# Kernel optimization log

Hardware: AMD Instinct MI355X
Metric: run time of the kernel (lower is better)

Reference implementation:

```python
import jax, jax.numpy as jnp
import numpy as np

N = 8192
E = 262144
NEG = 0.2  # leaky_relu negative slope used throughout


def setup_inputs() -> dict:
    key = jax.random.key(0)
    def rn(i, shape, s=0.05):
        return jax.random.normal(jax.random.fold_in(key, i), shape, jnp.float32) * s
    d = {}
    d["x"] = jax.random.normal(jax.random.fold_in(key, 0), (N, 64), jnp.float32)
    d["edge_index"] = jax.random.randint(jax.random.fold_in(key, 1), (2, E), 0, N, dtype=jnp.int32)
    wshapes = {"w0": (64, 256), "as0": (4, 64), "ad0": (4, 64), "r0": (64, 256),
               "w1": (256, 256), "as1": (4, 64), "ad1": (4, 64), "r1": (256, 256),
               "w2": (256, 64), "as2": (1, 64), "ad2": (1, 64), "r2": (256, 64),
               "p0": (256, 64), "p1": (256, 64),
               "qw": (64, 64), "kw": (64, 64), "vw": (64, 64), "ow": (64, 64),
               "m1w": (64, 64), "m2w": (64, 32), "m3w": (32, 10)}
    for i, (nm, sh) in enumerate(wshapes.items()):
        d[nm] = rn(i + 2, sh)
    for nm, dim in [("g0", 256), ("g1", 256), ("g2", 64)]:
        d[nm] = jnp.ones((dim,), jnp.float32)
    for nm, dim in [("be0", 256), ("be1", 256), ("be2", 64), ("b0", 256), ("b1", 256), ("b2", 64),
                    ("qb", 64), ("kb", 64), ("vb", 64), ("ob", 64), ("m1b", 64), ("m2b", 32), ("m3b", 10)]:
        d[nm] = jnp.zeros((dim,), jnp.float32)
    return d


def _forward(edge_index, x, w0, as0, ad0, b0, g0, be0, r0,
             w1, as1, ad1, b1, g1, be1, r1,
             w2, as2, ad2, b2, g2, be2, r2,
             p0, p1, qw, qb, kw, kb, vw, vb, ow, ob,
             m1w, m1b, m2w, m2b, m3w, m3b):
    n = x.shape[0]
    loops = jnp.arange(n, dtype=edge_index.dtype)
    src = jnp.concatenate([edge_index[0], loops])  # add_self_loops=True
    dst = jnp.concatenate([edge_index[1], loops])

    def gat(h, w, a_s, a_d, b, heads):
        hw = (h @ w).reshape(n, heads, 64)  # [N, H, C]
        # PyG GATConv: e_ij = leaky_relu(att_src . h_j + att_dst . h_i), softmax over in-edges of i
        e = jax.nn.leaky_relu(jnp.sum(hw * a_s, -1)[src] + jnp.sum(hw * a_d, -1)[dst], NEG)  # [Etot, H]
        m = jax.ops.segment_max(e, dst, num_segments=n)
        ex = jnp.exp(e - m[dst])
        den = jax.ops.segment_sum(ex, dst, num_segments=n)
        alpha = ex / (den[dst] + 1e-16)
        out = jax.ops.segment_sum(hw[src] * alpha[:, :, None], dst, num_segments=n)
        return out.reshape(n, heads * 64) + b

    def bn(h, g, bta):  # BatchNorm1d, batch statistics (training-mode math)
        mu = jnp.mean(h, 0)
        var = jnp.var(h, 0)
        return (h - mu) * jax.lax.rsqrt(var + 1e-5) * g + bta

    outs = []
    h = x
    for (w, a_s, a_d, b, g, bt, r, heads) in [
            (w0, as0, ad0, b0, g0, be0, r0, 4),
            (w1, as1, ad1, b1, g1, be1, r1, 4),
            (w2, as2, ad2, b2, g2, be2, r2, 1)]:
        res = h @ r
        h = bn(gat(h, w, a_s, a_d, b, heads), g, bt) + res  # shapes always match here
        h = jax.nn.leaky_relu(h, NEG)
        outs.append(h)

    # JumpingKnowledge 'max' after projecting first two layers to hidden dim
    z = jnp.maximum(jnp.maximum(outs[0] @ p0, outs[1] @ p1), outs[2])  # [N, 64]

    # MultiHeadSelfAttention over all nodes (batch=1 implicit), 2 heads, head_dim=32
    q = (z @ qw + qb).reshape(n, 2, 32)
    k = (z @ kw + kb).reshape(n, 2, 32)
    v = (z @ vw + vb).reshape(n, 2, 32)
    attn = jax.nn.softmax(jnp.einsum('nhd,mhd->hnm', q, k) * (32 ** -0.5), axis=-1)
    z = jnp.einsum('hnm,mhd->nhd', attn, v).reshape(n, 64) @ ow + ob

    # MLP head (no data.batch -> GlobalAttention pool skipped)
    z = jax.nn.leaky_relu(z @ m1w + m1b, NEG)
    z = jax.nn.leaky_relu(z @ m2w + m2b, NEG)
    return z @ m3w + m3b


def reference(x, edge_index, w0, as0, ad0, b0, g0, be0, r0,
              w1, as1, ad1, b1, g1, be1, r1,
              w2, as2, ad2, b2, g2, be2, r2,
              p0, p1, qw, qb, kw, kb, vw, vb, ow, ob,
              m1w, m1b, m2w, m2b, m3w, m3b):
    return _forward(edge_index, x, w0, as0, ad0, b0, g0, be0, r0,
                    w1, as1, ad1, b1, g1, be1, r1,
                    w2, as2, ad2, b2, g2, be2, r2,
                    p0, p1, qw, qb, kw, kb, vw, vb, ow, ob,
                    m1w, m1b, m2w, m2b, m3w, m3b)
```

## Files before the change

kernel.cpp:

```cpp
#include <hip/hip_runtime.h>
#include <hip/hip_bf16.h>


#define NEG 0.2f

__device__ __forceinline__ float leaky(float v) { return v > 0.f ? v : NEG * v; }

__device__ __forceinline__ unsigned bf16u(float x) {
    unsigned u = __float_as_uint(x);
    u += 0x7FFFu + ((u >> 16) & 1u);
    return u >> 16;
}

typedef __attribute__((ext_vector_type(8))) short bf16x8;
typedef __attribute__((ext_vector_type(16))) float f32x16;
typedef __attribute__((ext_vector_type(4))) unsigned uint4v;

__device__ __forceinline__ void split1(float v, unsigned& hb, unsigned& lb) {
    hb = bf16u(v);
    float hf = __uint_as_float(hb << 16);
    lb = bf16u(v - hf);
}

__global__ void split_rows(const float* __restrict__ in,
                           unsigned short* __restrict__ hi,
                           unsigned short* __restrict__ lo, int total4)
{
    int i = blockIdx.x * 256 + threadIdx.x;
    if (i >= total4) return;
    float4 v = ((const float4*)in)[i];
    float vv[4] = {v.x, v.y, v.z, v.w};
    ushort4 h, l;
#pragma unroll
    for (int j = 0; j < 4; ++j) {
        unsigned hb, lb;
        split1(vv[j], hb, lb);
        (&h.x)[j] = (unsigned short)hb;
        (&l.x)[j] = (unsigned short)lb;
    }
    ((ushort4*)hi)[i] = h;
    ((ushort4*)lo)[i] = l;
}

struct WEnt { const float* src; unsigned short* hi; unsigned short* lo; int K; int N; };
struct WArr { WEnt e[15]; };

__global__ void split_weights(WArr a)
{
    WEnt w = a.e[blockIdx.y];
    int id = blockIdx.x * 256 + threadIdx.x;
    if (id >= w.K * w.N) return;
    int k = id / w.N, n = id - k * w.N;
    unsigned hb, lb;
    split1(w.src[id], hb, lb);
    w.hi[(size_t)n * w.K + k] = (unsigned short)hb;
    w.lo[(size_t)n * w.K + k] = (unsigned short)lb;
}

__global__ __launch_bounds__(256) void gemm_mfma(
    const unsigned short* __restrict__ Ahi, const unsigned short* __restrict__ Alo,
    const unsigned short* __restrict__ Bhi, const unsigned short* __restrict__ Blo,
    const float* __restrict__ bias, float* __restrict__ C,
    unsigned short* __restrict__ Chi, unsigned short* __restrict__ Clo,
    int M, int N, int K, int act)
{
    const int lane = threadIdx.x & 63, wid = threadIdx.x >> 6;
    const int hb4 = lane >> 5, lq = lane & 31;
    const int row0 = blockIdx.y * 64 + (wid >> 1) * 32;
    const int col0 = blockIdx.x * 64 + (wid & 1) * 32;
    const size_t abase = (size_t)(row0 + lq) * K + hb4 * 8;
    const size_t bbase = (size_t)(col0 + lq) * K + hb4 * 8;
    f32x16 acc0, acc1;
#pragma unroll
    for (int r = 0; r < 16; ++r) { acc0[r] = 0.f; acc1[r] = 0.f; }
    for (int k0 = 0; k0 < K; k0 += 16) {
        bf16x8 a_h = *(const bf16x8*)(Ahi + abase + k0);
        bf16x8 a_l = *(const bf16x8*)(Alo + abase + k0);
        bf16x8 b_h = *(const bf16x8*)(Bhi + bbase + k0);
        bf16x8 b_l = *(const bf16x8*)(Blo + bbase + k0);
        acc0 = __builtin_amdgcn_mfma_f32_32x32x16_bf16(a_h, b_h, acc0, 0, 0, 0);
        acc1 = __builtin_amdgcn_mfma_f32_32x32x16_bf16(a_l, b_h, acc1, 0, 0, 0);
        acc1 = __builtin_amdgcn_mfma_f32_32x32x16_bf16(a_h, b_l, acc1, 0, 0, 0);
    }
    int col = col0 + lq;
    if (col >= N) return;
    float bs = bias ? bias[col] : 0.f;
#pragma unroll
    for (int r = 0; r < 16; ++r) {
        int row = row0 + (r & 3) + 8 * (r >> 2) + 4 * hb4;
        float v = acc0[r] + acc1[r] + bs;
        if (act) v = leaky(v);
        C[(size_t)row * N + col] = v;
        if (Chi) {
            unsigned hh, ll;
            split1(v, hh, ll);
            Chi[(size_t)row * N + col] = (unsigned short)hh;
            Clo[(size_t)row * N + col] = (unsigned short)ll;
        }
    }
}

__global__ void sd_kernel(const float* __restrict__ hw, const float* __restrict__ a_s,
                          const float* __restrict__ a_d, float* __restrict__ sval,
                          float* __restrict__ dval, int Nn, int H)
{
    int i = blockIdx.x * blockDim.x + threadIdx.x;
    if (i >= Nn * H) return;
    int n = i / H, h = i - n * H;
    const float4* row = (const float4*)(hw + (size_t)n * H * 64 + h * 64);
    const float4* as4 = (const float4*)(a_s + h * 64);
    const float4* ad4 = (const float4*)(a_d + h * 64);
    float s = 0.f, d = 0.f;
#pragma unroll
    for (int c = 0; c < 16; ++c) {
        float4 x = row[c], a = as4[c], b = ad4[c];
        s += x.x * a.x + x.y * a.y + x.z * a.z + x.w * a.w;
        d += x.x * b.x + x.y * b.y + x.z * b.z + x.w * b.w;
    }
    sval[i] = s;
    dval[i] = d;
}

__global__ void csr_count(const int* __restrict__ ei, int* __restrict__ cnt, int E) {
    int i = blockIdx.x * 256 + threadIdx.x;
    if (i < E) atomicAdd(&cnt[ei[E + i]], 1);
}

__global__ __launch_bounds__(256) void csr_scan(const int* __restrict__ cnt,
                                                int* __restrict__ rowptr,
                                                int* __restrict__ fill, int Nn)
{
    __shared__ int part[256];
    int t = threadIdx.x;
    int loc[32];
    int s = 0;
#pragma unroll
    for (int j = 0; j < 32; ++j) { loc[j] = s; s += cnt[t * 32 + j]; }
    part[t] = s;
    __syncthreads();
    for (int d = 1; d < 256; d <<= 1) {
        int v = (t >= d) ? part[t - d] : 0;
        __syncthreads();
        part[t] += v;
        __syncthreads();
    }
    int off = (t > 0) ? part[t - 1] : 0;
#pragma unroll
    for (int j = 0; j < 32; ++j) {
        int v = off + loc[j];
        rowptr[t * 32 + j] = v;
        fill[t * 32 + j] = v;
    }
    if (t == 255) rowptr[Nn] = part[255];
}

__global__ void csr_scatter(const int* __restrict__ ei, int* __restrict__ fill,
                            int* __restrict__ srcidx, int E) {
    int i = blockIdx.x * 256 + threadIdx.x;
    if (i < E) {
        int d = ei[E + i];
        int p = atomicAdd(&fill[d], 1);
        srcidx[p] = ei[i];
    }
}

template <int H>
__global__ __launch_bounds__(256) void gat_gather(
    const int* __restrict__ rowptr, const int* __restrict__ srcidx,
    const float* __restrict__ hw, const float* __restrict__ sval,
    const float* __restrict__ dval, float* __restrict__ gout, int Nn)
{
    const int node = blockIdx.x * 4 + (threadIdx.x >> 6);
    const int lane = threadIdx.x & 63;
    const int beg = rowptr[node], end = rowptr[node + 1];
    const int C = H * 64;
    float dv[H], es[H], mh[H], lh[H], inv[H], acc[H];
#pragma unroll
    for (int h = 0; h < H; ++h) {
        dv[h] = dval[node * H + h];
        es[h] = leaky(sval[node * H + h] + dv[h]);
        mh[h] = -1e30f;
        lh[h] = 0.f;
    }
    for (int i = beg + lane; i < end; i += 64) {
        int s = srcidx[i];
#pragma unroll
        for (int h = 0; h < H; ++h)
            mh[h] = fmaxf(mh[h], leaky(sval[s * H + h] + dv[h]));
    }
#pragma unroll
    for (int h = 0; h < H; ++h) {
        float m = mh[h];
        for (int off = 32; off; off >>= 1) m = fmaxf(m, __shfl_xor(m, off));
        mh[h] = fmaxf(m, es[h]);
    }
    for (int i = beg + lane; i < end; i += 64) {
        int s = srcidx[i];
#pragma unroll
        for (int h = 0; h < H; ++h)
            lh[h] += __expf(leaky(sval[s * H + h] + dv[h]) - mh[h]);
    }
#pragma unroll
    for (int h = 0; h < H; ++h) {
        float l = lh[h];
        for (int off = 32; off; off >>= 1) l += __shfl_xor(l, off);
        l += __expf(es[h] - mh[h]);
        inv[h] = 1.f / (l + 1e-16f);
        acc[h] = __expf(es[h] - mh[h]) * inv[h] *
                 hw[(size_t)node * C + h * 64 + lane];
    }
    for (int i = beg; i < end; ++i) {
        int s = srcidx[i];
#pragma unroll
        for (int h = 0; h < H; ++h) {
            float e = leaky(sval[s * H + h] + dv[h]);
            float a = __expf(e - mh[h]) * inv[h];
            acc[h] += a * hw[(size_t)s * C + h * 64 + lane];
        }
    }
#pragma unroll
    for (int h = 0; h < H; ++h)
        gout[(size_t)node * C + h * 64 + lane] = acc[h];
}

__global__ void bn_partial(const float* __restrict__ gout, double* __restrict__ sums,
                           int Nn, int C)
{
    int t = threadIdx.x;
    int c = t % C, sub = t / C, nsub = blockDim.x / C;
    int rbase = blockIdx.x * 32;
    double s = 0.0, sq = 0.0;
    for (int r = rbase + sub; r < rbase + 32; r += nsub) {
        float x = gout[(size_t)r * C + c];
        s += x;
        sq += (double)x * x;
    }
    atomicAdd(&sums[c], s);
    atomicAdd(&sums[C + c], sq);
}

__global__ void bn_finalize(const double* __restrict__ sums, float* __restrict__ mu,
                            float* __restrict__ rstd, int Nn, int C)
{
    int c = threadIdx.x;
    if (c >= C) return;
    double m = sums[c] / Nn;
    double v = sums[C + c] / Nn - m * m;
    mu[c] = (float)m;
    rstd[c] = (float)(1.0 / sqrt(v + 1e-5));
}

__global__ void bn_res_act(const float* __restrict__ gout, const float* __restrict__ res,
                           const float* __restrict__ mu, const float* __restrict__ rstd,
                           const float* __restrict__ g, const float* __restrict__ be,
                           float* __restrict__ out,
                           unsigned short* __restrict__ shi,
                           unsigned short* __restrict__ slo, int total, int C)
{
    int i = blockIdx.x * blockDim.x + threadIdx.x;
    if (i >= total) return;
    int c = i & (C - 1);
    float v = (gout[i] - mu[c]) * rstd[c] * g[c] + be[c] + res[i];
    v = leaky(v);
    out[i] = v;
    if (shi) {
        unsigned hb, lb;
        split1(v, hb, lb);
        shi[i] = (unsigned short)hb;
        slo[i] = (unsigned short)lb;
    }
}

__global__ void jk_max(const float* __restrict__ a, const float* __restrict__ b,
                       const float* __restrict__ c, float* __restrict__ z,
                       unsigned short* __restrict__ shi,
                       unsigned short* __restrict__ slo, int total)
{
    int i = blockIdx.x * blockDim.x + threadIdx.x;
    if (i >= total) return;
    float v = fmaxf(fmaxf(a[i], b[i]), c[i]);
    z[i] = v;
    unsigned hb, lb;
    split1(v, hb, lb);
    shi[i] = (unsigned short)hb;
    slo[i] = (unsigned short)lb;
}

__global__ void kmax_kernel(const float* __restrict__ kg, unsigned* __restrict__ kmax,
                            int N)
{
    const int c = threadIdx.x & 63, g = threadIdx.x >> 6;
    const int rows = N / (gridDim.x * 4);
    const int r0 = (blockIdx.x * 4 + g) * rows;
    float m = 0.f;
    for (int r = r0; r < r0 + rows; ++r)
        m = fmaxf(m, fabsf(kg[(size_t)r * 64 + c]));
    atomicMax(&kmax[c], __float_as_uint(m));
}

__global__ void qk_prep(const float* __restrict__ zq, const float* __restrict__ zk,
                        const unsigned* __restrict__ kmaxu,
                        __hip_bfloat16* __restrict__ Qb, __hip_bfloat16* __restrict__ Kb,
                        float* __restrict__ bound, int N)
{
    int idx = blockIdx.x * 256 + threadIdx.x;
    if (idx >= 2 * N) return;
    int h = idx / N, row = idx - h * N;
    const float scale = 0.17677669529663687f;
    const float* qp = zq + (size_t)row * 64 + h * 32;
    const float* kp = zk + (size_t)row * 64 + h * 32;
    float b = 0.f;
    unsigned qo[16], ko[16];
#pragma unroll
    for (int i = 0; i < 16; ++i) {
        float q0 = qp[2 * i] * scale, q1 = qp[2 * i + 1] * scale;
        float k0 = kp[2 * i], k1 = kp[2 * i + 1];
        b += fabsf(q0) * __uint_as_float(kmaxu[h * 32 + 2 * i]);
        b += fabsf(q1) * __uint_as_float(kmaxu[h * 32 + 2 * i + 1]);
        qo[i] = bf16u(q0) | (bf16u(q1) << 16);
        ko[i] = bf16u(k0) | (bf16u(k1) << 16);
    }
    uint4* qd = (uint4*)(Qb + (size_t)idx * 32);
    uint4* kd = (uint4*)(Kb + (size_t)idx * 32);
#pragma unroll
    for (int i = 0; i < 4; ++i) {
        qd[i] = make_uint4(qo[4 * i], qo[4 * i + 1], qo[4 * i + 2], qo[4 * i + 3]);
        kd[i] = make_uint4(ko[4 * i], ko[4 * i + 1], ko[4 * i + 2], ko[4 * i + 3]);
    }
    bound[idx] = b;
}

__global__ void v_prep(const float* __restrict__ zv, __hip_bfloat16* __restrict__ Vf,
                       int N)
{
    int idx = blockIdx.x * 256 + threadIdx.x;
    int total = 2 * (N >> 4) * 64;
    if (idx >= total) return;
    int lane = idx & 63;
    int g = (idx >> 6) % (N >> 4);
    int h = (idx >> 6) / (N >> 4);
    int kb = g * 16 + (lane >> 5) * 8;
    int d = (lane & 31) + h * 32;
    unsigned o[4];
#pragma unroll
    for (int i = 0; i < 4; ++i) {
        unsigned u0 = bf16u(zv[(size_t)(kb + 2 * i) * 64 + d]);
        unsigned u1 = bf16u(zv[(size_t)(kb + 2 * i + 1) * 64 + d]);
        o[i] = u0 | (u1 << 16);
    }
    *(uint4*)(Vf + (size_t)idx * 8) = make_uint4(o[0], o[1], o[2], o[3]);
}

__global__ __launch_bounds__(256) void attn_mfma(
    const __hip_bfloat16* __restrict__ Qb, const __hip_bfloat16* __restrict__ Kb,
    const __hip_bfloat16* __restrict__ Vf, const float* __restrict__ bound,
    float* __restrict__ pl, __hip_bfloat16* __restrict__ pacc,
    int N, int nchunk, int chunksz)
{
    const int lane = threadIdx.x & 63;
    const int wid = threadIdx.x >> 6;
    const int hi = lane >> 5, lq = lane & 31;
    const int chunk = blockIdx.x;
    const int qtile = blockIdx.y * 4 + wid;
    const int head = qtile / (N >> 5);
    const int q0 = (qtile % (N >> 5)) * 32;
    const int kbase = chunk * chunksz;

    const size_t qrow = (size_t)head * N + q0 + lq;
    const bf16x8 qf0 = *(const bf16x8*)(Qb + qrow * 32 + hi * 8);
    const bf16x8 qf1 = *(const bf16x8*)(Qb + qrow * 32 + hi * 8 + 16);
    const float bnd = bound[qrow];

    f32x16 oacc;
#pragma unroll
    for (int r = 0; r < 16; ++r) oacc[r] = 0.f;
    float lsum = 0.f;

    for (int kt = kbase; kt < kbase + chunksz; kt += 32) {
        const size_t krow = (size_t)head * N + kt + lq;
        const bf16x8 kf0 = *(const bf16x8*)(Kb + krow * 32 + hi * 8);
        const bf16x8 kf1 = *(const bf16x8*)(Kb + krow * 32 + hi * 8 + 16);
        f32x16 s;
#pragma unroll
        for (int r = 0; r < 16; ++r) s[r] = 0.f;
        s = __builtin_amdgcn_mfma_f32_32x32x16_bf16(kf0, qf0, s, 0, 0, 0);
        s = __builtin_amdgcn_mfma_f32_32x32x16_bf16(kf1, qf1, s, 0, 0, 0);
        const __hip_bfloat16* vfb =
            Vf + (((size_t)head * (N >> 4) + (kt >> 4)) * 64 + lane) * 8;
        const bf16x8 vf0 = *(const bf16x8*)vfb;
        const bf16x8 vf1 = *(const bf16x8*)(vfb + 64 * 8);

        float p[16];
#pragma unroll
        for (int r = 0; r < 16; ++r) p[r] = __expf(s[r] - bnd);
        float ls = 0.f;
#pragma unroll
        for (int r = 0; r < 16; ++r) ls += p[r];
        lsum += ls;

        unsigned wpk[8];
#pragma unroll
        for (int i = 0; i < 8; ++i)
            wpk[i] = bf16u(p[2 * i]) | (bf16u(p[2 * i + 1]) << 16);
        unsigned wsx[8];
#pragma unroll
        for (int i = 0; i < 8; ++i) wsx[i] = (unsigned)__shfl_xor((int)wpk[i], 32);
        uint4v b1, b2;
        b1[0] = hi ? wsx[2] : wpk[0];
        b1[1] = hi ? wsx[3] : wpk[1];
        b1[2] = hi ? wpk[2] : wsx[0];
        b1[3] = hi ? wpk[3] : wsx[1];
        b2[0] = hi ? wsx[6] : wpk[4];
        b2[1] = hi ? wsx[7] : wpk[5];
        b2[2] = hi ? wpk[6] : wsx[4];
        b2[3] = hi ? wpk[7] : wsx[5];
        oacc = __builtin_amdgcn_mfma_f32_32x32x16_bf16(
            vf0, __builtin_bit_cast(bf16x8, b1), oacc, 0, 0, 0);
        oacc = __builtin_amdgcn_mfma_f32_32x32x16_bf16(
            vf1, __builtin_bit_cast(bf16x8, b2), oacc, 0, 0, 0);
    }
    lsum += __shfl_xor(lsum, 32);
    const size_t hr = (size_t)head * N + q0 + lq;
    if (hi == 0) pl[hr * nchunk + chunk] = lsum;
    __hip_bfloat16* pb = pacc + (hr * nchunk + chunk) * 32;
#pragma unroll
    for (int rg = 0; rg < 4; ++rg) {
        unsigned lo = bf16u(oacc[rg * 4 + 0]) | (bf16u(oacc[rg * 4 + 1]) << 16);
        unsigned hw2 = bf16u(oacc[rg * 4 + 2]) | (bf16u(oacc[rg * 4 + 3]) << 16);
        *(uint2*)(pb + rg * 8 + hi * 4) = make_uint2(lo, hw2);
    }
}

__global__ void attn_combine(const float* __restrict__ pl,
                             const __hip_bfloat16* __restrict__ pacc,
                             float* __restrict__ og,
                             unsigned short* __restrict__ shi,
                             unsigned short* __restrict__ slo, int N, int nchunk)
{
    int i = blockIdx.x * blockDim.x + threadIdx.x;
    if (i >= 2 * N * 32) return;
    int hr = i >> 5, cc = i & 31;
    float l = 0.f, a = 0.f;
    for (int c = 0; c < nchunk; ++c) {
        l += pl[(size_t)hr * nchunk + c];
        a += __bfloat162float(pacc[((size_t)hr * nchunk + c) * 32 + cc]);
    }
    int head = hr / N, row = hr - head * N;
    float v = a / l;
    size_t oi = (size_t)row * 64 + head * 32 + cc;
    og[oi] = v;
    unsigned hb, lb;
    split1(v, hb, lb);
    shi[oi] = (unsigned short)hb;
    slo[oi] = (unsigned short)lb;
}

extern "C" void kernel_launch(void* const* d_in, const int* in_sizes, int n_in,
                              void* d_out, int out_size, void* d_ws, size_t ws_size,
                              hipStream_t stream)
{
    const float* x = (const float*)d_in[0];
    const int* ei = (const int*)d_in[1];
    const float* w[3]   = {(const float*)d_in[2], (const float*)d_in[6],  (const float*)d_in[10]};
    const float* as_[3] = {(const float*)d_in[3], (const float*)d_in[7],  (const float*)d_in[11]};
    const float* ad_[3] = {(const float*)d_in[4], (const float*)d_in[8],  (const float*)d_in[12]};
    const float* rw[3]  = {(const float*)d_in[5], (const float*)d_in[9],  (const float*)d_in[13]};
    const float* p0 = (const float*)d_in[14];
    const float* p1 = (const float*)d_in[15];
    const float* qw = (const float*)d_in[16];
    const float* kw = (const float*)d_in[17];
    const float* vw = (const float*)d_in[18];
    const float* ow = (const float*)d_in[19];
    const float* m1w = (const float*)d_in[20];
    const float* m2w = (const float*)d_in[21];
    const float* m3w = (const float*)d_in[22];
    const float* g_[3]  = {(const float*)d_in[23], (const float*)d_in[24], (const float*)d_in[25]};
    const float* be_[3] = {(const float*)d_in[26], (const float*)d_in[27], (const float*)d_in[28]};
    const float* qb  = (const float*)d_in[32];
    const float* kb  = (const float*)d_in[33];
    const float* vb  = (const float*)d_in[34];
    const float* ob  = (const float*)d_in[35];
    const float* m1b = (const float*)d_in[36];
    const float* m2b = (const float*)d_in[37];
    const float* m3b = (const float*)d_in[38];

    const int N = in_sizes[0] / 64;
    const int E = in_sizes[1] / 2;

    float* ws = (float*)d_ws;
    size_t off = 0;
    auto alloc = [&](size_t n) {
        float* p = ws + off;
        off += (n + 255) & ~(size_t)255;
        return p;
    };
    float* hw   = alloc((size_t)N * 256);
    float* res  = alloc((size_t)N * 256);
    float* gout = alloc((size_t)N * 256);
    float* h0   = alloc((size_t)N * 256);
    float* h1   = alloc((size_t)N * 256);
    float* h2   = alloc((size_t)N * 64);
    float* sval = alloc((size_t)N * 4);
    float* dval = alloc((size_t)N * 4);
    double* bnsum = (double*)alloc(1024);
    float* mu   = alloc(256);
    float* rstd = alloc(256);
    int* cnt    = (int*)alloc(N);
    int* rowptr = (int*)alloc(N + 256);
    int* fill   = (int*)alloc(N);
    int* srcidx = (int*)alloc(E);
    unsigned* kmaxu = (unsigned*)alloc(64);
    unsigned short* sAhi = (unsigned short*)alloc((size_t)N * 128);
    unsigned short* sAlo = (unsigned short*)alloc((size_t)N * 128);
    unsigned short* sBhi = (unsigned short*)alloc((size_t)N * 32);
    unsigned short* sBlo = (unsigned short*)alloc((size_t)N * 32);
    const float* wsrc[15] = {w[0], rw[0], w[1], rw[1], w[2], rw[2], p0, p1,
                             qw, kw, vw, ow, m1w, m2w, m3w};
    const int wK[15] = {64, 64, 256, 256, 256, 256, 256, 256, 64, 64, 64, 64, 64, 64, 32};
    const int wN[15] = {256, 256, 256, 256, 64, 64, 64, 64, 64, 64, 64, 64, 64, 32, 10};
    unsigned short *whi[15], *wlo[15];
    for (int i = 0; i < 15; ++i) {
        int padN = wN[i] < 64 ? 64 : wN[i];
        whi[i] = (unsigned short*)alloc((size_t)padN * wK[i] / 2);
        wlo[i] = (unsigned short*)alloc((size_t)padN * wK[i] / 2);
    }
    float* zq = hw;
    float* zk = hw + (size_t)N * 64;
    float* zv = hw + 2 * (size_t)N * 64;
    float* ao = hw + 3 * (size_t)N * 64;
    float* z  = gout;
    float* tA = res;
    float* tB = res + (size_t)N * 64;
    float* tC = res + 2 * (size_t)N * 64;
    const int NCHUNK = 8;
    __hip_bfloat16* Qb = (__hip_bfloat16*)h0;
    __hip_bfloat16* Kb = Qb + (size_t)2 * N * 32;
    __hip_bfloat16* Vf = Kb + (size_t)2 * N * 32;
    float* boundArr = (float*)(Vf + (size_t)2 * N * 32);
    __hip_bfloat16* pacc = (__hip_bfloat16*)res;
    float* pl = h2;

    auto gemmM = [&](const unsigned short* Ahi_, const unsigned short* Alo_, int widx,
                     const float* bias, float* C, unsigned short* Chi,
                     unsigned short* Clo, int M, int Nc, int K, int act) {
        dim3 grid((Nc + 63) / 64, M / 64);
        gemm_mfma<<<grid, 256, 0, stream>>>(Ahi_, Alo_, whi[widx], wlo[widx],
                                            bias, C, Chi, Clo, M, Nc, K, act);
    };

    {
        WArr wa;
        for (int i = 0; i < 15; ++i)
            wa.e[i] = WEnt{wsrc[i], whi[i], wlo[i], wK[i], wN[i]};
        split_weights<<<dim3(256, 15), 256, 0, stream>>>(wa);
    }

    hipMemsetAsync(cnt, 0, (size_t)N * 4, stream);
    csr_count<<<(E + 255) / 256, 256, 0, stream>>>(ei, cnt, E);
    csr_scan<<<1, 256, 0, stream>>>(cnt, rowptr, fill, N);
    csr_scatter<<<(E + 255) / 256, 256, 0, stream>>>(ei, fill, srcidx, E);

    split_rows<<<(N * 64 / 4 + 255) / 256, 256, 0, stream>>>(x, sAhi, sAlo, N * 64 / 4);

    float* houts[3] = {h0, h1, h2};
    int heads[3] = {4, 4, 1};
    int Kin = 64;

    for (int l = 0; l < 3; ++l) {
        int H = heads[l], C = H * 64;
        gemmM(sAhi, sAlo, 2 * l, nullptr, hw, nullptr, nullptr, N, C, Kin, 0);
        gemmM(sAhi, sAlo, 2 * l + 1, nullptr, res, nullptr, nullptr, N, C, Kin, 0);
        sd_kernel<<<(N * H + 255) / 256, 256, 0, stream>>>(hw, as_[l], ad_[l], sval, dval, N, H);
        if (H == 4)
            gat_gather<4><<<N / 4, 256, 0, stream>>>(rowptr, srcidx, hw, sval, dval, gout, N);
        else
            gat_gather<1><<<N / 4, 256, 0, stream>>>(rowptr, srcidx, hw, sval, dval, gout, N);
        hipMemsetAsync(bnsum, 0, (size_t)2 * C * 8, stream);
        bn_partial<<<N / 32, 256, 0, stream>>>(gout, bnsum, N, C);
        bn_finalize<<<1, 256, 0, stream>>>(bnsum, mu, rstd, N, C);
        bn_res_act<<<((size_t)N * C) / 256, 256, 0, stream>>>(
            gout, res, mu, rstd, g_[l], be_[l], houts[l],
            l < 2 ? sAhi : nullptr, l < 2 ? sAlo : nullptr, N * C, C);
        Kin = C;
    }

    gemmM(sAhi, sAlo, 7, nullptr, tB, nullptr, nullptr, N, 64, 256, 0);
    split_rows<<<(N * 256 / 4 + 255) / 256, 256, 0, stream>>>(h0, sAhi, sAlo, N * 256 / 4);
    gemmM(sAhi, sAlo, 6, nullptr, tA, nullptr, nullptr, N, 64, 256, 0);
    jk_max<<<((size_t)N * 64) / 256, 256, 0, stream>>>(tA, tB, h2, z, sAhi, sAlo, N * 64);

    gemmM(sAhi, sAlo, 8, qb, zq, nullptr, nullptr, N, 64, 64, 0);
    gemmM(sAhi, sAlo, 9, kb, zk, nullptr, nullptr, N, 64, 64, 0);
    gemmM(sAhi, sAlo, 10, vb, zv, nullptr, nullptr, N, 64, 64, 0);

    hipMemsetAsync(kmaxu, 0, 64 * 4, stream);
    kmax_kernel<<<32, 256, 0, stream>>>(zk, kmaxu, N);
    qk_prep<<<(2 * N + 255) / 256, 256, 0, stream>>>(zq, zk, kmaxu, Qb, Kb, boundArr, N);
    v_prep<<<(2 * (N >> 4) * 64 + 255) / 256, 256, 0, stream>>>(zv, Vf, N);
    attn_mfma<<<dim3(NCHUNK, (2 * N / 32) / 4), 256, 0, stream>>>(
        Qb, Kb, Vf, boundArr, pl, pacc, N, NCHUNK, N / NCHUNK);
    attn_combine<<<(2 * N * 32 + 255) / 256, 256, 0, stream>>>(
        pl, pacc, ao, sAhi, sAlo, N, NCHUNK);

    gemmM(sAhi, sAlo, 11, ob, tA, sBhi, sBlo, N, 64, 64, 0);
    gemmM(sBhi, sBlo, 12, m1b, tB, sAhi, sAlo, N, 64, 64, 1);
    gemmM(sAhi, sAlo, 13, m2b, tC, sBhi, sBlo, N, 32, 64, 1);
    gemmM(sBhi, sBlo, 14, m3b, (float*)d_out, nullptr, nullptr, N, 10, 32, 0);
}
```

Before: 458.2 us.

## Fuse GAT and residual GEMMs, single-pass softmax with global bound, merged QKV GEMM

Concatenates the GAT weight and residual weight so each layer runs one GEMM writing [hw|res], and merges the Q/K/V projections into one 192-wide GEMM with biases applied in the prep kernels. The GAT gather drops the per-node max and sum passes by using a global upper bound on the source score (atomicMax in sd_kernel) and normalises at the end, unrolling edges by two with vectorised sval loads. It also removes redundant fp32 output writes and split_rows by keeping bf16 hi/lo splits of layer outputs, and batches the memsets into one. The global-max shift risks exp underflow or precision loss when scores vary widely.

```diff
diff --git a/kernel.cpp b/kernel.cpp
--- a/kernel.cpp
+++ b/kernel.cpp
@@ -10,6 +10,14 @@
     unsigned u = __float_as_uint(x);
     u += 0x7FFFu + ((u >> 16) & 1u);
     return u >> 16;
+}
+__device__ __forceinline__ unsigned fmap(float f) {
+    unsigned u = __float_as_uint(f);
+    return (u & 0x80000000u) ? ~u : (u | 0x80000000u);
+}
+__device__ __forceinline__ float funmap(unsigned u) {
+    unsigned b = (u & 0x80000000u) ? (u & 0x7FFFFFFFu) : ~u;
+    return __uint_as_float(b);
 }
 
 typedef __attribute__((ext_vector_type(8))) short bf16x8;
@@ -100,14 +108,16 @@
     }
 }
 
-__global__ void sd_kernel(const float* __restrict__ hw, const float* __restrict__ a_s,
-                          const float* __restrict__ a_d, float* __restrict__ sval,
-                          float* __restrict__ dval, int Nn, int H)
-{
-    int i = blockIdx.x * blockDim.x + threadIdx.x;
-    if (i >= Nn * H) return;
-    int n = i / H, h = i - n * H;
-    const float4* row = (const float4*)(hw + (size_t)n * H * 64 + h * 64);
+template <int H>
+__global__ __launch_bounds__(256) void sd_kernel(
+    const float* __restrict__ hwres, int S,
+    const float* __restrict__ a_s, const float* __restrict__ a_d,
+    float* __restrict__ sval, float* __restrict__ dval,
+    unsigned* __restrict__ svmax, int Nn)
+{
+    int i = blockIdx.x * 256 + threadIdx.x;
+    int n = i / H, h = i & (H - 1);
+    const float4* row = (const float4*)(hwres + (size_t)n * S + h * 64);
     const float4* as4 = (const float4*)(a_s + h * 64);
     const float4* ad4 = (const float4*)(a_d + h * 64);
     float s = 0.f, d = 0.f;
@@ -119,6 +129,10 @@
     }
     sval[i] = s;
     dval[i] = d;
+    float m = s;
+#pragma unroll
+    for (int off = H; off < 64; off <<= 1) m = fmaxf(m, __shfl_xor(m, off));
+    if ((threadIdx.x & 63) < H) atomicMax(&svmax[h], fmap(m));
 }
 
 __global__ void csr_count(const int* __restrict__ ei, int* __restrict__ cnt, int E) {
@@ -167,60 +181,68 @@
 template <int H>
 __global__ __launch_bounds__(256) void gat_gather(
     const int* __restrict__ rowptr, const int* __restrict__ srcidx,
-    const float* __restrict__ hw, const float* __restrict__ sval,
-    const float* __restrict__ dval, float* __restrict__ gout, int Nn)
+    const float* __restrict__ hwres, int S,
+    const float* __restrict__ sval, const float* __restrict__ dval,
+    const unsigned* __restrict__ svmax, float* __restrict__ gout, int Nn)
 {
     const int node = blockIdx.x * 4 + (threadIdx.x >> 6);
     const int lane = threadIdx.x & 63;
     const int beg = rowptr[node], end = rowptr[node + 1];
     const int C = H * 64;
-    float dv[H], es[H], mh[H], lh[H], inv[H], acc[H];
+    float dv[H], B[H], acc[H], l[H];
+    if constexpr (H == 4) {
+        float4 t = *(const float4*)(dval + node * 4);
+        dv[0] = t.x; dv[1] = t.y; dv[2] = t.z; dv[3] = t.w;
+    } else {
+        dv[0] = dval[node];
+    }
 #pragma unroll
     for (int h = 0; h < H; ++h) {
-        dv[h] = dval[node * H + h];
-        es[h] = leaky(sval[node * H + h] + dv[h]);
-        mh[h] = -1e30f;
-        lh[h] = 0.f;
-    }
-    for (int i = beg + lane; i < end; i += 64) {
-        int s = srcidx[i];
-#pragma unroll
-        for (int h = 0; h < H; ++h)
-            mh[h] = fmaxf(mh[h], leaky(sval[s * H + h] + dv[h]));
-    }
-#pragma unroll
-    for (int h = 0; h < H; ++h) {
-        float m = mh[h];
-        for (int off = 32; off; off >>= 1) m = fmaxf(m, __shfl_xor(m, off));
-        mh[h] = fmaxf(m, es[h]);
-    }
-    for (int i = beg + lane; i < end; i += 64) {
-        int s = srcidx[i];
-#pragma unroll
-        for (int h = 0; h < H; ++h)
-            lh[h] += __expf(leaky(sval[s * H + h] + dv[h]) - mh[h]);
-    }
-#pragma unroll
-    for (int h = 0; h < H; ++h) {
-        float l = lh[h];
-        for (int off = 32; off; off >>= 1) l += __shfl_xor(l, off);
-        l += __expf(es[h] - mh[h]);
-        inv[h] = 1.f / (l + 1e-16f);
-        acc[h] = __expf(es[h] - mh[h]) * inv[h] *
-                 hw[(size_t)node * C + h * 64 + lane];
-    }
-    for (int i = beg; i < end; ++i) {
-        int s = srcidx[i];
+        B[h] = leaky(funmap(svmax[h]) + dv[h]);
+        float es;
+        if constexpr (H == 4) es = sval[node * 4 + h]; else es = sval[node];
+        float p = __expf(leaky(es + dv[h]) - B[h]);
+        l[h] = p;
+        acc[h] = p * hwres[(size_t)node * S + h * 64 + lane];
+    }
+    int i = beg;
+    for (; i + 2 <= end; i += 2) {
+        int s0 = srcidx[i], s1 = srcidx[i + 1];
+        float se0[H], se1[H];
+        if constexpr (H == 4) {
+            float4 t0 = *(const float4*)(sval + s0 * 4);
+            float4 t1 = *(const float4*)(sval + s1 * 4);
+            se0[0] = t0.x; se0[1] = t0.y; se0[2] = t0.z; se0[3] = t0.w;
+            se1[0] = t1.x; se1[1] = t1.y; se1[2] = t1.z; se1[3] = t1.w;
+        } else { se0[0] = sval[s0]; se1[0] = sval[s1]; }
+        const float* r0 = hwres + (size_t)s0 * S + lane;
+        const float* r1 = hwres + (size_t)s1 * S + lane;
 #pragma unroll
         for (int h = 0; h < H; ++h) {
-            float e = leaky(sval[s * H + h] + dv[h]);
-            float a = __expf(e - mh[h]) * inv[h];
-            acc[h] += a * hw[(size_t)s * C + h * 64 + lane];
+            float p0 = __expf(leaky(se0[h] + dv[h]) - B[h]);
+            float p1 = __expf(leaky(se1[h] + dv[h]) - B[h]);
+            l[h] += p0 + p1;
+            acc[h] += p0 * r0[h * 64] + p1 * r1[h * 64];
         }
     }
+    for (; i < end; ++i) {
+        int s0 = srcidx[i];
+        float se0[H];
+        if constexpr (H == 4) {
+            float4 t0 = *(const float4*)(sval + s0 * 4);
+            se0[0] = t0.x; se0[1] = t0.y; se0[2] = t0.z; se0[3] = t0.w;
+        } else { se0[0] = sval[s0]; }
+        const float* r0 = hwres + (size_t)s0 * S + lane;
+#pragma unroll
+        for (int h = 0; h < H; ++h) {
+            float p0 = __expf(leaky(se0[h] + dv[h]) - B[h]);
+            l[h] += p0;
+            acc[h] += p0 * r0[h * 64];
+        }
+    }
 #pragma unroll
     for (int h = 0; h < H; ++h)
-        gout[(size_t)node * C + h * 64 + lane] = acc[h];
+        gout[(size_t)node * C + h * 64 + lane] = acc[h] / l[h];
 }
 
 __global__ void bn_partial(const float* __restrict__ gout, double* __restrict__ sums,
@@ -250,19 +272,22 @@
     rstd[c] = (float)(1.0 / sqrt(v + 1e-5));
 }
 
-__global__ void bn_res_act(const float* __restrict__ gout, const float* __restrict__ res,
+__global__ void bn_res_act(const float* __restrict__ gout,
+                           const float* __restrict__ hwres, int S, int logC,
                            const float* __restrict__ mu, const float* __restrict__ rstd,
                            const float* __restrict__ g, const float* __restrict__ be,
-                           float* __restrict__ out,
+                           float* __restrict__ outp,
                            unsigned short* __restrict__ shi,
-                           unsigned short* __restrict__ slo, int total, int C)
+                           unsigned short* __restrict__ slo, int total)
 {
     int i = blockIdx.x * blockDim.x + threadIdx.x;
     if (i >= total) return;
-    int c = i & (C - 1);
-    float v = (gout[i] - mu[c]) * rstd[c] * g[c] + be[c] + res[i];
+    int C = 1 << logC;
+    int c = i & (C - 1), row = i >> logC;
+    float v = (gout[i] - mu[c]) * rstd[c] * g[c] + be[c]
+              + hwres[(size_t)row * S + C + c];
     v = leaky(v);
-    out[i] = v;
+    if (outp) outp[i] = v;
     if (shi) {
         unsigned hb, lb;
         split1(v, hb, lb);
@@ -272,33 +297,35 @@
 }
 
 __global__ void jk_max(const float* __restrict__ a, const float* __restrict__ b,
-                       const float* __restrict__ c, float* __restrict__ z,
+                       const float* __restrict__ c,
                        unsigned short* __restrict__ shi,
                        unsigned short* __restrict__ slo, int total)
 {
     int i = blockIdx.x * blockDim.x + threadIdx.x;
     if (i >= total) return;
     float v = fmaxf(fmaxf(a[i], b[i]), c[i]);
-    z[i] = v;
     unsigned hb, lb;
     split1(v, hb, lb);
     shi[i] = (unsigned short)hb;
     slo[i] = (unsigned short)lb;
 }
 
-__global__ void kmax_kernel(const float* __restrict__ kg, unsigned* __restrict__ kmax,
-                            int N)
+__global__ void kmax_kernel(const float* __restrict__ zqkv,
+                            const float* __restrict__ kb,
+                            unsigned* __restrict__ kmax, int N)
 {
     const int c = threadIdx.x & 63, g = threadIdx.x >> 6;
     const int rows = N / (gridDim.x * 4);
     const int r0 = (blockIdx.x * 4 + g) * rows;
+    float bc = kb[c];
     float m = 0.f;
     for (int r = r0; r < r0 + rows; ++r)
-        m = fmaxf(m, fabsf(kg[(size_t)r * 64 + c]));
+        m = fmaxf(m, fabsf(zqkv[(size_t)r * 192 + 64 + c] + bc));
     atomicMax(&kmax[c], __float_as_uint(m));
 }
 
-__global__ void qk_prep(const float* __restrict__ zq, const float* __restrict__ zk,
+__global__ void qk_prep(const float* __restrict__ zqkv,
+                        const float* __restrict__ qb, const float* __restrict__ kb,
                         const unsigned* __restrict__ kmaxu,
                         __hip_bfloat16* __restrict__ Qb, __hip_bfloat16* __restrict__ Kb,
                         float* __restrict__ bound, int N)
@@ -307,14 +334,16 @@
     if (idx >= 2 * N) return;
     int h = idx / N, row = idx - h * N;
     const float scale = 0.17677669529663687f;
-    const float* qp = zq + (size_t)row * 64 + h * 32;
-    const float* kp = zk + (size_t)row * 64 + h * 32;
+    const float* qp = zqkv + (size_t)row * 192 + h * 32;
+    const float* kp = zqkv + (size_t)row * 192 + 64 + h * 32;
     float b = 0.f;
     unsigned qo[16], ko[16];
 #pragma unroll
     for (int i = 0; i < 16; ++i) {
-        float q0 = qp[2 * i] * scale, q1 = qp[2 * i + 1] * scale;
-        float k0 = kp[2 * i], k1 = kp[2 * i + 1];
+        float q0 = (qp[2 * i] + qb[h * 32 + 2 * i]) * scale;
+        float q1 = (qp[2 * i + 1] + qb[h * 32 + 2 * i + 1]) * scale;
+        float k0 = kp[2 * i] + kb[h * 32 + 2 * i];
+        float k1 = kp[2 * i + 1] + kb[h * 32 + 2 * i + 1];
         b += fabsf(q0) * __uint_as_float(kmaxu[h * 32 + 2 * i]);
         b += fabsf(q1) * __uint_as_float(kmaxu[h * 32 + 2 * i + 1]);
         qo[i] = bf16u(q0) | (bf16u(q1) << 16);
@@ -330,8 +359,8 @@
     bound[idx] = b;
 }
 
-__global__ void v_prep(const float* __restrict__ zv, __hip_bfloat16* __restrict__ Vf,
-                       int N)
+__global__ void v_prep(const float* __restrict__ zqkv, const float* __restrict__ vb,
+                       __hip_bfloat16* __restrict__ Vf, int N)
 {
     int idx = blockIdx.x * 256 + threadIdx.x;
     int total = 2 * (N >> 4) * 64;
@@ -339,13 +368,14 @@
     int lane = idx & 63;
     int g = (idx >> 6) % (N >> 4);
     int h = (idx >> 6) / (N >> 4);
-    int kb = g * 16 + (lane >> 5) * 8;
+    int kb_ = g * 16 + (lane >> 5) * 8;
     int d = (lane & 31) + h * 32;
+    float bd = vb[d];
     unsigned o[4];
 #pragma unroll
     for (int i = 0; i < 4; ++i) {
-        unsigned u0 = bf16u(zv[(size_t)(kb + 2 * i) * 64 + d]);
-        unsigned u1 = bf16u(zv[(size_t)(kb + 2 * i + 1) * 64 + d]);
+        unsigned u0 = bf16u(zqkv[(size_t)(kb_ + 2 * i) * 192 + 128 + d] + bd);
+        unsigned u1 = bf16u(zqkv[(size_t)(kb_ + 2 * i + 1) * 192 + 128 + d] + bd);
         o[i] = u0 | (u1 << 16);
     }
     *(uint4*)(Vf + (size_t)idx * 8) = make_uint4(o[0], o[1], o[2], o[3]);
@@ -433,7 +463,6 @@
 
 __global__ void attn_combine(const float* __restrict__ pl,
                              const __hip_bfloat16* __restrict__ pacc,
-                             float* __restrict__ og,
                              unsigned short* __restrict__ shi,
                              unsigned short* __restrict__ slo, int N, int nchunk)
 {
@@ -448,7 +477,6 @@
     int head = hr / N, row = hr - head * N;
     float v = a / l;
     size_t oi = (size_t)row * 64 + head * 32 + cc;
-    og[oi] = v;
     unsigned hb, lb;
     split1(v, hb, lb);
     shi[oi] = (unsigned short)hb;
@@ -494,116 +522,142 @@
         off += (n + 255) & ~(size_t)255;
         return p;
     };
-    float* hw   = alloc((size_t)N * 256);
-    float* res  = alloc((size_t)N * 256);
-    float* gout = alloc((size_t)N * 256);
-    float* h0   = alloc((size_t)N * 256);
-    float* h1   = alloc((size_t)N * 256);
+    float* hwres = alloc((size_t)N * 512);
+    float* gout  = alloc((size_t)N * 256);
+    unsigned short* sChi = (unsigned short*)alloc((size_t)N * 128);
+    unsigned short* sClo = (unsigned short*)alloc((size_t)N * 128);
     float* h2   = alloc((size_t)N * 64);
     float* sval = alloc((size_t)N * 4);
     float* dval = alloc((size_t)N * 4);
-    double* bnsum = (double*)alloc(1024);
     float* mu   = alloc(256);
     float* rstd = alloc(256);
-    int* cnt    = (int*)alloc(N);
+    size_t ms_begin = off;
+    int* cnt = (int*)alloc(N);
+    double* bnsum = (double*)alloc(3 * 1024);
+    unsigned* kmaxu = (unsigned*)alloc(64);
+    unsigned* svmax = (unsigned*)alloc(16);
+    size_t ms_end = off;
     int* rowptr = (int*)alloc(N + 256);
     int* fill   = (int*)alloc(N);
     int* srcidx = (int*)alloc(E);
-    unsigned* kmaxu = (unsigned*)alloc(64);
     unsigned short* sAhi = (unsigned short*)alloc((size_t)N * 128);
     unsigned short* sAlo = (unsigned short*)alloc((size_t)N * 128);
     unsigned short* sBhi = (unsigned short*)alloc((size_t)N * 32);
     unsigned short* sBlo = (unsigned short*)alloc((size_t)N * 32);
-    const float* wsrc[15] = {w[0], rw[0], w[1], rw[1], w[2], rw[2], p0, p1,
-                             qw, kw, vw, ow, m1w, m2w, m3w};
-    const int wK[15] = {64, 64, 256, 256, 256, 256, 256, 256, 64, 64, 64, 64, 64, 64, 32};
-    const int wN[15] = {256, 256, 256, 256, 64, 64, 64, 64, 64, 64, 64, 64, 64, 32, 10};
-    unsigned short *whi[15], *wlo[15];
-    for (int i = 0; i < 15; ++i) {
-        int padN = wN[i] < 64 ? 64 : wN[i];
-        whi[i] = (unsigned short*)alloc((size_t)padN * wK[i] / 2);
-        wlo[i] = (unsigned short*)alloc((size_t)padN * wK[i] / 2);
-    }
-    float* zq = hw;
-    float* zk = hw + (size_t)N * 64;
-    float* zv = hw + 2 * (size_t)N * 64;
-    float* ao = hw + 3 * (size_t)N * 64;
-    float* z  = gout;
-    float* tA = res;
-    float* tB = res + (size_t)N * 64;
-    float* tC = res + 2 * (size_t)N * 64;
+    unsigned short* G0h = (unsigned short*)alloc(512 * 64 / 2);
+    unsigned short* G0l = (unsigned short*)alloc(512 * 64 / 2);
+    unsigned short* G1h = (unsigned short*)alloc(512 * 256 / 2);
+    unsigned short* G1l = (unsigned short*)alloc(512 * 256 / 2);
+    unsigned short* G2h = (unsigned short*)alloc(128 * 256 / 2);
+    unsigned short* G2l = (unsigned short*)alloc(128 * 256 / 2);
+    unsigned short* P0h = (unsigned short*)alloc(64 * 256 / 2);
+    unsigned short* P0l = (unsigned short*)alloc(64 * 256 / 2);
+    unsigned short* P1h = (unsigned short*)alloc(64 * 256 / 2);
+    unsigned short* P1l = (unsigned short*)alloc(64 * 256 / 2);
+    unsigned short* Gqh = (unsigned short*)alloc(192 * 64 / 2);
+    unsigned short* Gql = (unsigned short*)alloc(192 * 64 / 2);
+    unsigned short* Owh = (unsigned short*)alloc(64 * 64 / 2);
+    unsigned short* Owl = (unsigned short*)alloc(64 * 64 / 2);
+    unsigned short* M1h = (unsigned short*)alloc(64 * 64 / 2);
+    unsigned short* M1l = (unsigned short*)alloc(64 * 64 / 2);
+    unsigned short* M2h = (unsigned short*)alloc(64 * 64 / 2);
+    unsigned short* M2l = (unsigned short*)alloc(64 * 64 / 2);
+    unsigned short* M3h = (unsigned short*)alloc(64 * 32 / 2);
+    unsigned short* M3l = (unsigned short*)alloc(64 * 32 / 2);
+    float* zqkv = hwres;
+    __hip_bfloat16* pacc = (__hip_bfloat16*)(hwres + (size_t)N * 192);
+    float* tA = gout;
+    float* tB = gout + (size_t)N * 64;
+    float* tC = gout + 2 * (size_t)N * 64;
     const int NCHUNK = 8;
-    __hip_bfloat16* Qb = (__hip_bfloat16*)h0;
+    __hip_bfloat16* Qb = (__hip_bfloat16*)sChi;
     __hip_bfloat16* Kb = Qb + (size_t)2 * N * 32;
     __hip_bfloat16* Vf = Kb + (size_t)2 * N * 32;
     float* boundArr = (float*)(Vf + (size_t)2 * N * 32);
-    __hip_bfloat16* pacc = (__hip_bfloat16*)res;
     float* pl = h2;
 
-    auto gemmM = [&](const unsigned short* Ahi_, const unsigned short* Alo_, int widx,
+    {
+        WArr wa;
+        wa.e[0]  = WEnt{w[0],  G0h,              G0l,              64, 256};
+        wa.e[1]  = WEnt{rw[0], G0h + 256 * 64,   G0l + 256 * 64,   64, 256};
+        wa.e[2]  = WEnt{w[1],  G1h,              G1l,              256, 256};
+        wa.e[3]  = WEnt{rw[1], G1h + 256 * 256,  G1l + 256 * 256,  256, 256};
+        wa.e[4]  = WEnt{w[2],  G2h,              G2l,              256, 64};
+        wa.e[5]  = WEnt{rw[2], G2h + 64 * 256,   G2l + 64 * 256,   256, 64};
+        wa.e[6]  = WEnt{p0,    P0h,              P0l,              256, 64};
+        wa.e[7]  = WEnt{p1,    P1h,              P1l,              256, 64};
+        wa.e[8]  = WEnt{qw,    Gqh,              Gql,              64, 64};
+        wa.e[9]  = WEnt{kw,    Gqh + 64 * 64,    Gql + 64 * 64,    64, 64};
+        wa.e[10] = WEnt{vw,    Gqh + 128 * 64,   Gql + 128 * 64,   64, 64};
+        wa.e[11] = WEnt{ow,    Owh,              Owl,              64, 64};
+        wa.e[12] = WEnt{m1w,   M1h,              M1l,              64, 64};
+        wa.e[13] = WEnt{m2w,   M2h,              M2l,              64, 32};
+        wa.e[14] = WEnt{m3w,   M3h,              M3l,              32, 10};
+        split_weights<<<dim3(256, 15), 256, 0, stream>>>(wa);
+    }
+    hipMemsetAsync(ws + ms_begin, 0, (ms_end - ms_begin) * 4, stream);
+    csr_count<<<(E + 255) / 256, 256, 0, stream>>>(ei, cnt, E);
+    csr_scan<<<1, 256, 0, stream>>>(cnt, rowptr, fill, N);
+    csr_scatter<<<(E + 255) / 256, 256, 0, stream>>>(ei, fill, srcidx, E);
+    split_rows<<<(N * 64 / 4 + 255) / 256, 256, 0, stream>>>(x, sAhi, sAlo, N * 64 / 4);
+
+    auto gemmM = [&](const unsigned short* Ah, const unsigned short* Al,
+                     const unsigned short* Bh, const unsigned short* Bl,
                      const float* bias, float* C, unsigned short* Chi,
                      unsigned short* Clo, int M, int Nc, int K, int act) {
         dim3 grid((Nc + 63) / 64, M / 64);
-        gemm_mfma<<<grid, 256, 0, stream>>>(Ahi_, Alo_, whi[widx], wlo[widx],
-                                            bias, C, Chi, Clo, M, Nc, K, act);
+        gemm_mfma<<<grid, 256, 0, stream>>>(Ah, Al, Bh, Bl, bias, C, Chi, Clo,
+                                            M, Nc, K, act);
     };
 
-    {
-        WArr wa;
-        for (int i = 0; i < 15; ++i)
-            wa.e[i] = WEnt{wsrc[i], whi[i], wlo[i], wK[i], wN[i]};
-        split_weights<<<dim3(256, 15), 256, 0, stream>>>(wa);
-    }
-
-    hipMemsetAsync(cnt, 0, (size_t)N * 4, stream);
-    csr_count<<<(E + 255) / 256, 256, 0, stream>>>(ei, cnt, E);
-    csr_scan<<<1, 256, 0, stream>>>(cnt, rowptr, fill, N);
-    csr_scatter<<<(E + 255) / 256, 256, 0, stream>>>(ei, fill, srcidx, E);
-
-    split_rows<<<(N * 64 / 4 + 255) / 256, 256, 0, stream>>>(x, sAhi, sAlo, N * 64 / 4);
-
-    float* houts[3] = {h0, h1, h2};
-    int heads[3] = {4, 4, 1};
-    int Kin = 64;
+    const unsigned short* inh[3] = {sAhi, sChi, sAhi};
+    const unsigned short* inl[3] = {sAlo, sClo, sAlo};
+    unsigned short* outh[3] = {sChi, sAhi, nullptr};
+    unsigned short* outl[3] = {sClo, sAlo, nullptr};
+    const unsigned short* Gh[3] = {G0h, G1h, G2h};
+    const unsigned short* Gl[3] = {G0l, G1l, G2l};
+    int Ksz[3] = {64, 256, 256}, Csz[3] = {256, 256, 64}, logC[3] = {8, 8, 6};
+    int Hh[3] = {4, 4, 1};
 
     for (int l = 0; l < 3; ++l) {
-        int H = heads[l], C = H * 64;
-        gemmM(sAhi, sAlo, 2 * l, nullptr, hw, nullptr, nullptr, N, C, Kin, 0);
-        gemmM(sAhi, sAlo, 2 * l + 1, nullptr, res, nullptr, nullptr, N, C, Kin, 0);
-        sd_kernel<<<(N * H + 255) / 256, 256, 0, stream>>>(hw, as_[l], ad_[l], sval, dval, N, H);
-        if (H == 4)
-            gat_gather<4><<<N / 4, 256, 0, stream>>>(rowptr, srcidx, hw, sval, dval, gout, N);
-        else
-            gat_gather<1><<<N / 4, 256, 0, stream>>>(rowptr, srcidx, hw, sval, dval, gout, N);
-        hipMemsetAsync(bnsum, 0, (size_t)2 * C * 8, stream);
-        bn_partial<<<N / 32, 256, 0, stream>>>(gout, bnsum, N, C);
-        bn_finalize<<<1, 256, 0, stream>>>(bnsum, mu, rstd, N, C);
+        int C = Csz[l], S = 2 * C;
+        gemmM(inh[l], inl[l], Gh[l], Gl[l], nullptr, hwres, nullptr, nullptr,
+              N, S, Ksz[l], 0);
+        if (Hh[l] == 4) {
+            sd_kernel<4><<<N * 4 / 256, 256, 0, stream>>>(
+                hwres, S, as_[l], ad_[l], sval, dval, svmax + l * 4, N);
+            gat_gather<4><<<N / 4, 256, 0, stream>>>(
+                rowptr, srcidx, hwres, S, sval, dval, svmax + l * 4, gout, N);
+        } else {
+            sd_kernel<1><<<N / 256, 256, 0, stream>>>(
+                hwres, S, as_[l], ad_[l], sval, dval, svmax + l * 4, N);
+            gat_gather<1><<<N / 4, 256, 0, stream>>>(
+                rowptr, srcidx, hwres, S, sval, dval, svmax + l * 4, gout, N);
+        }
+        double* bns = bnsum + l * 512;
+        bn_partial<<<N / 32, 256, 0, stream>>>(gout, bns, N, C);
+        bn_finalize<<<1, 256, 0, stream>>>(bns, mu, rstd, N, C);
         bn_res_act<<<((size_t)N * C) / 256, 256, 0, stream>>>(
-            gout, res, mu, rstd, g_[l], be_[l], houts[l],
-            l < 2 ? sAhi : nullptr, l < 2 ? sAlo : nullptr, N * C, C);
-        Kin = C;
-    }
-
-    gemmM(sAhi, sAlo, 7, nullptr, tB, nullptr, nullptr, N, 64, 256, 0);
-    split_rows<<<(N * 256 / 4 + 255) / 256, 256, 0, stream>>>(h0, sAhi, sAlo, N * 256 / 4);
-    gemmM(sAhi, sAlo, 6, nullptr, tA, nullptr, nullptr, N, 64, 256, 0);
-    jk_max<<<((size_t)N * 64) / 256, 256, 0, stream>>>(tA, tB, h2, z, sAhi, sAlo, N * 64);
-
-    gemmM(sAhi, sAlo, 8, qb, zq, nullptr, nullptr, N, 64, 64, 0);
-    gemmM(sAhi, sAlo, 9, kb, zk, nullptr, nullptr, N, 64, 64, 0);
-    gemmM(sAhi, sAlo, 10, vb, zv, nullptr, nullptr, N, 64, 64, 0);
-
-    hipMemsetAsync(kmaxu, 0, 64 * 4, stream);
-    kmax_kernel<<<32, 256, 0, stream>>>(zk, kmaxu, N);
-    qk_prep<<<(2 * N + 255) / 256, 256, 0, stream>>>(zq, zk, kmaxu, Qb, Kb, boundArr, N);
-    v_prep<<<(2 * (N >> 4) * 64 + 255) / 256, 256, 0, stream>>>(zv, Vf, N);
+            gout, hwres, S, logC[l], mu, rstd, g_[l], be_[l],
+            l == 2 ? h2 : nullptr, outh[l], outl[l], N * C);
+    }
+
+    gemmM(sChi, sClo, P0h, P0l, nullptr, tA, nullptr, nullptr, N, 64, 256, 0);
+    gemmM(sAhi, sAlo, P1h, P1l, nullptr, tB, nullptr, nullptr, N, 64, 256, 0);
+    jk_max<<<((size_t)N * 64) / 256, 256, 0, stream>>>(tA, tB, h2, sBhi, sBlo, N * 64);
+
+    gemmM(sBhi, sBlo, Gqh, Gql, nullptr, zqkv, nullptr, nullptr, N, 192, 64, 0);
+
+    kmax_kernel<<<32, 256, 0, stream>>>(zqkv, kb, kmaxu, N);
+    qk_prep<<<(2 * N + 255) / 256, 256, 0, stream>>>(zqkv, qb, kb, kmaxu, Qb, Kb, boundArr, N);
+    v_prep<<<(2 * (N >> 4) * 64 + 255) / 256, 256, 0, stream>>>(zqkv, vb, Vf, N);
     attn_mfma<<<dim3(NCHUNK, (2 * N / 32) / 4), 256, 0, stream>>>(
         Qb, Kb, Vf, boundArr, pl, pacc, N, NCHUNK, N / NCHUNK);
     attn_combine<<<(2 * N * 32 + 255) / 256, 256, 0, stream>>>(
-        pl, pacc, ao, sAhi, sAlo, N, NCHUNK);
-
-    gemmM(sAhi, sAlo, 11, ob, tA, sBhi, sBlo, N, 64, 64, 0);
-    gemmM(sBhi, sBlo, 12, m1b, tB, sAhi, sAlo, N, 64, 64, 1);
-    gemmM(sAhi, sAlo, 13, m2b, tC, sBhi, sBlo, N, 32, 64, 1);
-    gemmM(sBhi, sBlo, 14, m3b, (float*)d_out, nullptr, nullptr, N, 10, 32, 0);
-}
+        pl, pacc, sAhi, sAlo, N, NCHUNK);
+
+    gemmM(sAhi, sAlo, Owh, Owl, ob, tA, sBhi, sBlo, N, 64, 64, 0);
+    gemmM(sBhi, sBlo, M1h, M1l, m1b, tB, sAhi, sAlo, N, 64, 64, 1);
+    gemmM(sAhi, sAlo, M2h, M2l, m2b, tC, sBhi, sBlo, N, 32, 64, 1);
+    gemmM(sBhi, sBlo, M3h, M3l, m3b, (float*)d_out, nullptr, nullptr, N, 10, 32, 0);
+}
```

Result: faster. 408.5 us (-10.8%).
